# Kernel optimization log

Hardware: AMD Instinct MI355X
Metric: run time of the kernel (lower is better)

## Reference

```python
import jax, jax.numpy as jnp
import numpy as np

DIM = 64
N_EMBED = 1024
DECAY = 0.99
EPS = 1e-05
B, T = 2048, 128


def setup_inputs() -> dict:
    key = jax.random.key(0)
    k1, k2, k3 = jax.random.split(key, 3)
    x = jax.random.normal(k1, (B, T, DIM), dtype=jnp.float32)
    mask = jax.random.randint(k2, (B, T), 0, 2).astype(bool)
    embed = jax.random.normal(k3, (DIM, N_EMBED), dtype=jnp.float32)
    cluster_size = jnp.zeros((N_EMBED,), dtype=jnp.float32)
    embed_avg = embed  # buffer initialized as embed.clone()
    return {"input": x, "mask": mask, "embed": embed,
            "cluster_size": cluster_size, "embed_avg": embed_avg}


def reference(input, mask, embed, cluster_size, embed_avg):
    # --- nearest-codebook lookup ---
    flat = input.reshape(-1, DIM)                               # [N, D]
    dist = (jnp.sum(flat * flat, axis=1, keepdims=True)
            - 2.0 * flat @ embed
            + jnp.sum(embed * embed, axis=0, keepdims=True))    # [N, K]
    embed_ind = jnp.argmin(dist, axis=1)                        # [N]
    quantize = embed.T[embed_ind].reshape(input.shape)          # gather [N, D]
    # straight-through estimator
    quantize = input + jax.lax.stop_gradient(quantize - input)

    # --- masked MSE loss: mse over rows where ~mask, averaged over n_valid*DIM ---
    valid = (~mask).reshape(-1).astype(input.dtype)             # [N]
    n_valid = jnp.sum(valid)
    sq = jnp.sum((jax.lax.stop_gradient(quantize) - input).reshape(-1, DIM) ** 2, axis=1)
    loss = jnp.sum(sq * valid) / (n_valid * DIM)

    # --- EMA codebook update (training branch) ---
    counts = jnp.zeros((N_EMBED,), input.dtype).at[embed_ind].add(valid)
    embed_sum = jnp.zeros((N_EMBED, DIM), input.dtype).at[embed_ind].add(
        flat * valid[:, None]).T                                # [D, K]
    new_cluster_size = cluster_size * DECAY + (1.0 - DECAY) * counts
    new_embed_avg = embed_avg * DECAY + (1.0 - DECAY) * embed_sum
    total = jnp.sum(new_cluster_size)
    smoothed = (new_cluster_size + EPS) / (total + N_EMBED * EPS) * total
    new_embed = new_embed_avg / smoothed[None, :]
    return quantize, loss, new_embed, new_cluster_size, new_embed_avg
```

## Files before the change

### kernel.cpp

```cpp
#include <hip/hip_runtime.h>

typedef short short8 __attribute__((ext_vector_type(8)));
typedef float f32x16 __attribute__((ext_vector_type(16)));

#define DIMV   64
#define NEMB   1024
#define NROWS  262144
#define DECAYF 0.99f
#define OMDF   0.01f
#define EPSF   1e-5f
#define NSH    8

#define OQ   0
#define OL   16777216
#define OE   16777217
#define ONC  16842753
#define OA   16843777
#define OEH  16777216
#define OEL  (16777216 + 32768)

#define WS_E2     0
#define WS_CNT    1024
#define WS_ESUM   9216
#define WS_LOSSP  74752
#define WS_TOTAL  75776
#define WS_ET     75780
#define WS_KWV    141316
#define WS_BUCKET 272388

__device__ __forceinline__ unsigned short f2bf(float f) {
    unsigned u = __float_as_uint(f);
    u = u + 0x7FFFu + ((u >> 16) & 1u);
    return (unsigned short)(u >> 16);
}
__device__ __forceinline__ float bf2f(unsigned short h) {
    return __uint_as_float(((unsigned)h) << 16);
}

__global__ void vq_prep(const float* __restrict__ embed, float* __restrict__ et)
{
    int idx = blockIdx.x * 256 + threadIdx.x;
    int d = idx >> 10;
    int k = idx & (NEMB - 1);
    et[k * DIMV + d] = embed[idx];
}

__global__ void vq_e2(const float* __restrict__ et, float* __restrict__ e2)
{
    int k = blockIdx.x * 256 + threadIdx.x;
    const float4* ep = (const float4*)(et + k * DIMV);
    float s = 0.f;
    #pragma unroll
    for (int i = 0; i < 16; i++) {
        float4 v = ep[i];
        s = fmaf(v.x, v.x, fmaf(v.y, v.y, fmaf(v.z, v.z, fmaf(v.w, v.w, s))));
    }
    e2[k] = s;
}

__global__ void vq_prep_b(const float* __restrict__ embed,
                          unsigned short* __restrict__ eh,
                          unsigned short* __restrict__ el)
{
    int t = blockIdx.x * 256 + threadIdx.x;
    int j  = t & 7;
    int L  = (t >> 3) & 63;
    int s  = (t >> 9) & 3;
    int nt = t >> 11;
    int d    = s * 16 + (L >> 5) * 8 + j;
    int code = nt * 32 + (L & 31);
    float e = embed[d * NEMB + code];
    unsigned short hb = f2bf(e);
    eh[t] = hb;
    el[t] = f2bf(e - bf2f(hb));
}

__global__ __launch_bounds__(256, 2) void vq_main(
    const float* __restrict__ x, const int* __restrict__ mask,
    const unsigned short* __restrict__ eh, const unsigned short* __restrict__ el,
    const float* __restrict__ et, const float* __restrict__ e2g,
    float* __restrict__ out, unsigned short* __restrict__ kwv,
    float* __restrict__ loss_part)
{
    const int tid  = threadIdx.x;
    const int lane = tid & 63;
    const int wid  = tid >> 6;
    const int wbase = blockIdx.x * 256 + wid * 64;
    const int lm = lane & 31;
    const int lh = lane >> 5;

    __shared__ float lw[4];

    short8 ah[2][4], al[2][4];
    #pragma unroll
    for (int mt = 0; mt < 2; mt++) {
        const float* xr = x + (size_t)(wbase + mt * 32 + lm) * DIMV + lh * 8;
        #pragma unroll
        for (int s = 0; s < 4; s++) {
            const float* xp = xr + s * 16;
            #pragma unroll
            for (int j = 0; j < 8; j++) {
                float f = xp[j];
                unsigned short hb = f2bf(f);
                ah[mt][s][j] = (short)hb;
                al[mt][s][j] = (short)f2bf(f - bf2f(hb));
            }
        }
    }

    int b1[2][16], b2[2][16];
    #pragma unroll
    for (int mt = 0; mt < 2; mt++)
        #pragma unroll
        for (int r = 0; r < 16; r++) { b1[mt][r] = 0x7FFFFFFF; b2[mt][r] = 0x7FFFFFFF; }

    const short8* ehf = (const short8*)eh;
    const short8* elf = (const short8*)el;

    for (int nt = 0; nt < 32; nt++) {
        short8 bh[4], bl[4];
        #pragma unroll
        for (int s = 0; s < 4; s++) {
            bh[s] = ehf[(nt * 4 + s) * 64 + lane];
            bl[s] = elf[(nt * 4 + s) * 64 + lane];
        }
        const int   klane = nt * 32 + lm;
        const float e2s   = e2g[klane] * 2048.0f;

        f32x16 acc0, acc1;
        #pragma unroll
        for (int i = 0; i < 16; i++) { acc0[i] = 0.0f; acc1[i] = 0.0f; }

        #pragma unroll
        for (int s = 0; s < 4; s++) {
            acc0 = __builtin_amdgcn_mfma_f32_32x32x16_bf16(ah[0][s], bh[s], acc0, 0, 0, 0);
            acc1 = __builtin_amdgcn_mfma_f32_32x32x16_bf16(ah[1][s], bh[s], acc1, 0, 0, 0);
        }
        #pragma unroll
        for (int s = 0; s < 4; s++) {
            acc0 = __builtin_amdgcn_mfma_f32_32x32x16_bf16(ah[0][s], bl[s], acc0, 0, 0, 0);
            acc1 = __builtin_amdgcn_mfma_f32_32x32x16_bf16(ah[1][s], bl[s], acc1, 0, 0, 0);
        }
        #pragma unroll
        for (int s = 0; s < 4; s++) {
            acc0 = __builtin_amdgcn_mfma_f32_32x32x16_bf16(al[0][s], bh[s], acc0, 0, 0, 0);
            acc1 = __builtin_amdgcn_mfma_f32_32x32x16_bf16(al[1][s], bh[s], acc1, 0, 0, 0);
        }

        #pragma unroll
        for (int r = 0; r < 16; r++) {
            int q0   = (int)fmaf(acc0[r], -4096.0f, e2s);
            int key0 = (int)(((unsigned)q0) << 10) | klane;
            int lo0 = min(b1[0][r], key0), hi0 = max(b1[0][r], key0);
            b1[0][r] = lo0; b2[0][r] = min(b2[0][r], hi0);

            int q1   = (int)fmaf(acc1[r], -4096.0f, e2s);
            int key1 = (int)(((unsigned)q1) << 10) | klane;
            int lo1 = min(b1[1][r], key1), hi1 = max(b1[1][r], key1);
            b1[1][r] = lo1; b2[1][r] = min(b2[1][r], hi1);
        }
    }

    int sm1 = 0x7FFFFFFF, sm2 = 0x7FFFFFFF, sc = 1;
    unsigned long long hm = (lane < 32) ? 0xFFFFFFFFull : 0xFFFFFFFF00000000ull;
    #pragma unroll
    for (int mt = 0; mt < 2; mt++) {
        #pragma unroll
        for (int r = 0; r < 16; r++) {
            int v1 = b1[mt][r], v2 = b2[mt][r];
            #pragma unroll
            for (int m = 1; m <= 16; m <<= 1) {
                int o1 = __shfl_xor(v1, m, 64);
                int o2 = __shfl_xor(v2, m, 64);
                int lo = min(v1, o1), hi = max(v1, o1);
                v1 = lo;
                v2 = min(min(v2, o2), hi);
            }
            int thr = (v1 >> 10) + 41;
            bool in1 = (b1[mt][r] >> 10) <= thr;
            bool in2 = (b2[mt][r] >> 10) <= thr;
            unsigned long long B1 = __ballot(in1), B2 = __ballot(in2);
            int cnt = (int)__popcll(B1 & hm) + (int)__popcll(B2 & hm);
            int w1a = __shfl(v1, 0, 64),  w2a = __shfl(v2, 0, 64),  ca = __shfl(cnt, 0, 64);
            int w1b = __shfl(v1, 32, 64), w2b = __shfl(v2, 32, 64), cb = __shfl(cnt, 32, 64);
            int r0 = mt * 32 + (r & 3) + 8 * (r >> 2);
            if (lane == r0)     { sm1 = w1a; sm2 = w2a; sc = ca; }
            if (lane == r0 + 4) { sm1 = w1b; sm2 = w2b; sc = cb; }
        }
    }

    const int row = wbase + lane;
    int kw = sm1 & 1023;

    {
        unsigned long long fm = __ballot(sc >= 3);
        while (fm) {
            int j = __ffsll(fm) - 1; fm &= (fm - 1);
            const float4* xr = (const float4*)(x + (size_t)(wbase + j) * DIMV);
            float4 xb[16];
            float xb2 = 0.f;
            #pragma unroll
            for (int i = 0; i < 16; i++) {
                float4 v = xr[i];
                xb[i] = v;
                xb2 += v.x * v.x + v.y * v.y + v.z * v.z + v.w * v.w;
            }
            float bd = 3.4e38f; int bc = 0;
            for (int t = 0; t < 16; t++) {
                int c = lane + (t << 6);
                const float4* ep = (const float4*)(et + (c << 6));
                float ax = 0.f, ay = 0.f, az = 0.f, aw = 0.f;
                #pragma unroll 4
                for (int i = 0; i < 16; i++) {
                    float4 ev = ep[i];
                    ax = fmaf(xb[i].x, ev.x, ax);
                    ay = fmaf(xb[i].y, ev.y, ay);
                    az = fmaf(xb[i].z, ev.z, az);
                    aw = fmaf(xb[i].w, ev.w, aw);
                }
                float dot = (ax + ay) + (az + aw);
                float d = (xb2 - 2.0f * dot) + e2g[c];
                if (d < bd) { bd = d; bc = c; }
            }
            #pragma unroll
            for (int m = 1; m < 64; m <<= 1) {
                float od = __shfl_xor(bd, m, 64);
                int   oc = __shfl_xor(bc, m, 64);
                if (od < bd || (od == bd && oc < bc)) { bd = od; bc = oc; }
            }
            if (lane == j) kw = bc;
        }
    }

    float4 xv[16];
    {
        const float4* xp = (const float4*)(x + (size_t)row * DIMV);
        #pragma unroll
        for (int i = 0; i < 16; i++) xv[i] = xp[i];
    }

    if (sc == 2) {
        float x2 = 0.f;
        #pragma unroll
        for (int i = 0; i < 16; i++)
            x2 += xv[i].x * xv[i].x + xv[i].y * xv[i].y + xv[i].z * xv[i].z + xv[i].w * xv[i].w;

        auto fdist = [&](int k) -> float {
            const float4* ep = (const float4*)(et + (k << 6));
            float ax = 0.f, ay = 0.f, az = 0.f, aw = 0.f;
            #pragma unroll
            for (int i = 0; i < 16; i++) {
                float4 ev = ep[i];
                ax = fmaf(xv[i].x, ev.x, ax);
                ay = fmaf(xv[i].y, ev.y, ay);
                az = fmaf(xv[i].z, ev.z, az);
                aw = fmaf(xv[i].w, ev.w, aw);
            }
            float dot = (ax + ay) + (az + aw);
            return (x2 - 2.0f * dot) + e2g[k];
        };

        int k2 = sm2 & 1023;
        float d1 = fdist(kw);
        float d2 = fdist(k2);
        if (d2 < d1 || (d2 == d1 && k2 < kw)) kw = k2;
    }

    const bool valid = (mask[row] == 0);
    float sq = 0.f;
    float4* qp = (float4*)(out + OQ + (size_t)row * DIMV);
    const float4* erow = (const float4*)(et + (kw << 6));
    #pragma unroll
    for (int i = 0; i < 16; i++) {
        float4 xvv = xv[i];
        float4 ev  = erow[i];
        float q0 = xvv.x + (ev.x - xvv.x);
        float q1 = xvv.y + (ev.y - xvv.y);
        float q2 = xvv.z + (ev.z - xvv.z);
        float q3 = xvv.w + (ev.w - xvv.w);
        float4 q4 = {q0, q1, q2, q3};
        qp[i] = q4;
        float d0 = q0 - xvv.x, d1 = q1 - xvv.y, d2 = q2 - xvv.z, d3 = q3 - xvv.w;
        sq += d0 * d0 + d1 * d1 + d2 * d2 + d3 * d3;
    }

    kwv[row] = valid ? (unsigned short)kw : (unsigned short)0xFFFF;

    float v = valid ? sq : 0.0f;
    #pragma unroll
    for (int off = 32; off > 0; off >>= 1) v += __shfl_down(v, off, 64);
    if (lane == 0) lw[wid] = v;
    __syncthreads();
    if (tid == 0) loss_part[blockIdx.x] = (lw[0] + lw[1]) + (lw[2] + lw[3]);
}

__global__ __launch_bounds__(256) void vq_bucket(
    const unsigned short* __restrict__ kwv, const float* __restrict__ x,
    int* __restrict__ cnt, int* __restrict__ bucket,
    float* __restrict__ esum, int capS)
{
    int row = blockIdx.x * 256 + threadIdx.x;
    unsigned short c = kwv[row];
    if (c == 0xFFFFu) return;
    int s = blockIdx.x & (NSH - 1);
    int pos = atomicAdd(&cnt[(int)c + (s << 10)], 1);
    if (pos < capS) {
        bucket[((size_t)s * NEMB + (int)c) * capS + pos] = row;
    } else {
        const float* xr = x + (size_t)row * DIMV;
        float* ep = esum + ((int)c << 6);
        #pragma unroll 8
        for (int i = 0; i < DIMV; i++) atomicAdd(ep + i, xr[i]);
    }
}

__global__ __launch_bounds__(512) void vq_esum(
    const float* __restrict__ x, const int* __restrict__ cnt,
    const int* __restrict__ bucket, float* __restrict__ esum, int capS)
{
    const int tid  = threadIdx.x;
    const int lane = tid & 63;
    const int wid  = tid >> 6;
    const int c    = blockIdx.x;
    const int n    = min(cnt[c + (wid << 10)], capS);
    const int* bp  = bucket + ((size_t)wid * NEMB + c) * capS;
    __shared__ float part[8][64];

    float acc = 0.f;
    for (int i = 0; i < n; i += 8) {
        float tmp[8];
        if (i + 8 <= n) {
            int4 a = *(const int4*)(bp + i);
            int4 b = *(const int4*)(bp + i + 4);
            tmp[0] = x[(size_t)a.x * DIMV + lane];
            tmp[1] = x[(size_t)a.y * DIMV + lane];
            tmp[2] = x[(size_t)a.z * DIMV + lane];
            tmp[3] = x[(size_t)a.w * DIMV + lane];
            tmp[4] = x[(size_t)b.x * DIMV + lane];
            tmp[5] = x[(size_t)b.y * DIMV + lane];
            tmp[6] = x[(size_t)b.z * DIMV + lane];
            tmp[7] = x[(size_t)b.w * DIMV + lane];
        } else {
            #pragma unroll
            for (int k = 0; k < 8; k++) {
                int idx = i + k;
                tmp[k] = (idx < n) ? x[(size_t)bp[idx] * DIMV + lane] : 0.f;
            }
        }
        acc += ((tmp[0] + tmp[1]) + (tmp[2] + tmp[3]))
             + ((tmp[4] + tmp[5]) + (tmp[6] + tmp[7]));
    }

    part[wid][lane] = acc;
    __syncthreads();
    if (tid < 64) {
        float s = 0.f;
        #pragma unroll
        for (int w = 0; w < 8; w++) s += part[w][lane];
        esum[(c << 6) + lane] += s;
    }
}

__global__ __launch_bounds__(1024) void vq_finalA(
    const float* __restrict__ cluster_size, const int* __restrict__ cnt,
    const float* __restrict__ loss_part, float* __restrict__ out,
    float* __restrict__ total_ws)
{
    __shared__ float s1[1024];
    __shared__ float s2[1024];
    __shared__ float s3[1024];
    int k = threadIdx.x;
    int ci = 0;
    #pragma unroll
    for (int s = 0; s < NSH; s++) ci += cnt[k + (s << 10)];
    float c   = (float)ci;
    float ncs = cluster_size[k] * DECAYF + OMDF * c;
    out[ONC + k] = ncs;
    s1[k] = ncs; s2[k] = c; s3[k] = loss_part[k];
    __syncthreads();
    for (int off = 512; off > 0; off >>= 1) {
        if (k < off) { s1[k] += s1[k + off]; s2[k] += s2[k + off]; s3[k] += s3[k + off]; }
        __syncthreads();
    }
    if (k == 0) {
        total_ws[0] = s1[0];
        out[OL] = s3[0] / (s2[0] * (float)DIMV);
    }
}

__global__ void vq_finalB(const float* __restrict__ embed_avg,
                          const float* __restrict__ esum,
                          float* __restrict__ out,
                          const float* __restrict__ total_ws)
{
    int idx = blockIdx.x * 256 + threadIdx.x;
    int k = idx & (NEMB - 1);
    int d = idx >> 10;
    float avg = embed_avg[idx] * DECAYF + OMDF * esum[(k << 6) + d];
    out[OA + idx] = avg;
    float ncs   = out[ONC + k];
    float total = *total_ws;
    float sm = (ncs + EPSF) / (total + (float)NEMB * EPSF) * total;
    out[OE + idx] = avg / sm;
}

extern "C" void kernel_launch(void* const* d_in, const int* in_sizes, int n_in,
                              void* d_out, int out_size, void* d_ws, size_t ws_size,
                              hipStream_t stream)
{
    const float* x            = (const float*)d_in[0];
    const int*   mask         = (const int*)d_in[1];
    const float* embed        = (const float*)d_in[2];
    const float* cluster_size = (const float*)d_in[3];
    const float* embed_avg    = (const float*)d_in[4];
    float* out = (float*)d_out;
    float* ws  = (float*)d_ws;

    unsigned short* eh     = (unsigned short*)(out + OEH);
    unsigned short* el     = (unsigned short*)(out + OEL);
    unsigned short* kwv    = (unsigned short*)(ws + WS_KWV);
    int*            cnt    = (int*)(ws + WS_CNT);
    int*            bucket = (int*)(ws + WS_BUCKET);

    int capS = 0;
    size_t avail = ws_size / sizeof(float);
    if (avail > (size_t)WS_BUCKET) {
        size_t per = (avail - (size_t)WS_BUCKET) / ((size_t)NEMB * NSH);
        if (per > 768) per = 768;
        capS = (int)per & ~7;
    }

    hipMemsetAsync(ws + WS_CNT, 0, (size_t)(WS_LOSSP - WS_CNT) * sizeof(float), stream);

    vq_prep<<<65536 / 256, 256, 0, stream>>>(embed, ws + WS_ET);
    vq_e2<<<NEMB / 256, 256, 0, stream>>>(ws + WS_ET, ws + WS_E2);
    vq_prep_b<<<65536 / 256, 256, 0, stream>>>(embed, eh, el);
    vq_main<<<NROWS / 256, 256, 0, stream>>>(x, mask, eh, el, ws + WS_ET, ws + WS_E2,
                                             out, kwv, ws + WS_LOSSP);
    vq_bucket<<<NROWS / 256, 256, 0, stream>>>(kwv, x, cnt, bucket, ws + WS_ESUM, capS);
    vq_esum<<<NEMB, 512, 0, stream>>>(x, cnt, bucket, ws + WS_ESUM, capS);
    vq_finalA<<<1, 1024, 0, stream>>>(cluster_size, cnt, ws + WS_LOSSP,
                                      out, ws + WS_TOTAL);
    vq_finalB<<<65536 / 256, 256, 0, stream>>>(embed_avg, ws + WS_ESUM, out, ws + WS_TOTAL);
}
```

Baseline: 378.4 us.

## Halve rows per wave in vq_main to raise occupancy; fuse prep kernels

```diff
diff --git a/kernel.cpp b/kernel.cpp
--- a/kernel.cpp
+++ b/kernel.cpp
@@ -23,10 +23,10 @@
 #define WS_CNT    1024
 #define WS_ESUM   9216
 #define WS_LOSSP  74752
-#define WS_TOTAL  75776
-#define WS_ET     75780
-#define WS_KWV    141316
-#define WS_BUCKET 272388
+#define WS_TOTAL  76800
+#define WS_ET     76804
+#define WS_KWV    142340
+#define WS_BUCKET 273412
 
 __device__ __forceinline__ unsigned short f2bf(float f) {
     unsigned u = __float_as_uint(f);
@@ -37,45 +37,39 @@
     return __uint_as_float(((unsigned)h) << 16);
 }
 
-__global__ void vq_prep(const float* __restrict__ embed, float* __restrict__ et)
-{
-    int idx = blockIdx.x * 256 + threadIdx.x;
-    int d = idx >> 10;
-    int k = idx & (NEMB - 1);
-    et[k * DIMV + d] = embed[idx];
-}
-
-__global__ void vq_e2(const float* __restrict__ et, float* __restrict__ e2)
-{
-    int k = blockIdx.x * 256 + threadIdx.x;
-    const float4* ep = (const float4*)(et + k * DIMV);
-    float s = 0.f;
-    #pragma unroll
-    for (int i = 0; i < 16; i++) {
-        float4 v = ep[i];
-        s = fmaf(v.x, v.x, fmaf(v.y, v.y, fmaf(v.z, v.z, fmaf(v.w, v.w, s))));
-    }
-    e2[k] = s;
-}
-
-__global__ void vq_prep_b(const float* __restrict__ embed,
-                          unsigned short* __restrict__ eh,
-                          unsigned short* __restrict__ el)
+__global__ void vq_prep(const float* __restrict__ embed, float* __restrict__ et,
+                        unsigned short* __restrict__ eh, unsigned short* __restrict__ el)
 {
     int t = blockIdx.x * 256 + threadIdx.x;
+    int d = t >> 10;
+    int k = t & (NEMB - 1);
+    et[k * DIMV + d] = embed[t];
     int j  = t & 7;
     int L  = (t >> 3) & 63;
     int s  = (t >> 9) & 3;
     int nt = t >> 11;
-    int d    = s * 16 + (L >> 5) * 8 + j;
+    int db   = s * 16 + (L >> 5) * 8 + j;
     int code = nt * 32 + (L & 31);
-    float e = embed[d * NEMB + code];
+    float e = embed[db * NEMB + code];
     unsigned short hb = f2bf(e);
     eh[t] = hb;
     el[t] = f2bf(e - bf2f(hb));
 }
 
-__global__ __launch_bounds__(256, 2) void vq_main(
+__global__ void vq_e2(const float* __restrict__ et, float* __restrict__ e2)
+{
+    int k = blockIdx.x * 256 + threadIdx.x;
+    const float4* ep = (const float4*)(et + k * DIMV);
+    float s = 0.f;
+    #pragma unroll
+    for (int i = 0; i < 16; i++) {
+        float4 v = ep[i];
+        s = fmaf(v.x, v.x, fmaf(v.y, v.y, fmaf(v.z, v.z, fmaf(v.w, v.w, s))));
+    }
+    e2[k] = s;
+}
+
+__global__ __launch_bounds__(256, 5) void vq_main(
     const float* __restrict__ x, const int* __restrict__ mask,
     const unsigned short* __restrict__ eh, const unsigned short* __restrict__ el,
     const float* __restrict__ et, const float* __restrict__ e2g,
@@ -85,16 +79,15 @@
     const int tid  = threadIdx.x;
     const int lane = tid & 63;
     const int wid  = tid >> 6;
-    const int wbase = blockIdx.x * 256 + wid * 64;
+    const int wbase = blockIdx.x * 128 + wid * 32;
     const int lm = lane & 31;
     const int lh = lane >> 5;
 
     __shared__ float lw[4];
 
-    short8 ah[2][4], al[2][4];
-    #pragma unroll
-    for (int mt = 0; mt < 2; mt++) {
-        const float* xr = x + (size_t)(wbase + mt * 32 + lm) * DIMV + lh * 8;
+    short8 ah[4], al[4];
+    {
+        const float* xr = x + (size_t)(wbase + lm) * DIMV + lh * 8;
         #pragma unroll
         for (int s = 0; s < 4; s++) {
             const float* xp = xr + s * 16;
@@ -102,17 +95,15 @@
             for (int j = 0; j < 8; j++) {
                 float f = xp[j];
                 unsigned short hb = f2bf(f);
-                ah[mt][s][j] = (short)hb;
-                al[mt][s][j] = (short)f2bf(f - bf2f(hb));
-            }
-        }
-    }
-
-    int b1[2][16], b2[2][16];
-    #pragma unroll
-    for (int mt = 0; mt < 2; mt++)
-        #pragma unroll
-        for (int r = 0; r < 16; r++) { b1[mt][r] = 0x7FFFFFFF; b2[mt][r] = 0x7FFFFFFF; }
+                ah[s][j] = (short)hb;
+                al[s][j] = (short)f2bf(f - bf2f(hb));
+            }
+        }
+    }
+
+    int b1[16], b2[16];
+    #pragma unroll
+    for (int r = 0; r < 16; r++) { b1[r] = 0x7FFFFFFF; b2[r] = 0x7FFFFFFF; }
 
     const short8* ehf = (const short8*)eh;
     const short8* elf = (const short8*)el;
@@ -127,69 +118,54 @@
         const int   klane = nt * 32 + lm;
         const float e2s   = e2g[klane] * 2048.0f;
 
-        f32x16 acc0, acc1;
-        #pragma unroll
-        for (int i = 0; i < 16; i++) { acc0[i] = 0.0f; acc1[i] = 0.0f; }
-
-        #pragma unroll
-        for (int s = 0; s < 4; s++) {
-            acc0 = __builtin_amdgcn_mfma_f32_32x32x16_bf16(ah[0][s], bh[s], acc0, 0, 0, 0);
-            acc1 = __builtin_amdgcn_mfma_f32_32x32x16_bf16(ah[1][s], bh[s], acc1, 0, 0, 0);
-        }
-        #pragma unroll
-        for (int s = 0; s < 4; s++) {
-            acc0 = __builtin_amdgcn_mfma_f32_32x32x16_bf16(ah[0][s], bl[s], acc0, 0, 0, 0);
-            acc1 = __builtin_amdgcn_mfma_f32_32x32x16_bf16(ah[1][s], bl[s], acc1, 0, 0, 0);
-        }
-        #pragma unroll
-        for (int s = 0; s < 4; s++) {
-            acc0 = __builtin_amdgcn_mfma_f32_32x32x16_bf16(al[0][s], bh[s], acc0, 0, 0, 0);
-            acc1 = __builtin_amdgcn_mfma_f32_32x32x16_bf16(al[1][s], bh[s], acc1, 0, 0, 0);
-        }
+        f32x16 acc;
+        #pragma unroll
+        for (int i = 0; i < 16; i++) acc[i] = 0.0f;
+
+        #pragma unroll
+        for (int s = 0; s < 4; s++)
+            acc = __builtin_amdgcn_mfma_f32_32x32x16_bf16(ah[s], bh[s], acc, 0, 0, 0);
+        #pragma unroll
+        for (int s = 0; s < 4; s++)
+            acc = __builtin_amdgcn_mfma_f32_32x32x16_bf16(ah[s], bl[s], acc, 0, 0, 0);
+        #pragma unroll
+        for (int s = 0; s < 4; s++)
+            acc = __builtin_amdgcn_mfma_f32_32x32x16_bf16(al[s], bh[s], acc, 0, 0, 0);
 
         #pragma unroll
         for (int r = 0; r < 16; r++) {
-            int q0   = (int)fmaf(acc0[r], -4096.0f, e2s);
-            int key0 = (int)(((unsigned)q0) << 10) | klane;
-            int lo0 = min(b1[0][r], key0), hi0 = max(b1[0][r], key0);
-            b1[0][r] = lo0; b2[0][r] = min(b2[0][r], hi0);
-
-            int q1   = (int)fmaf(acc1[r], -4096.0f, e2s);
-            int key1 = (int)(((unsigned)q1) << 10) | klane;
-            int lo1 = min(b1[1][r], key1), hi1 = max(b1[1][r], key1);
-            b1[1][r] = lo1; b2[1][r] = min(b2[1][r], hi1);
+            int q   = (int)fmaf(acc[r], -4096.0f, e2s);
+            int key = (int)(((unsigned)q) << 10) | klane;
+            int lo = min(b1[r], key), hi = max(b1[r], key);
+            b1[r] = lo; b2[r] = min(b2[r], hi);
         }
     }
 
     int sm1 = 0x7FFFFFFF, sm2 = 0x7FFFFFFF, sc = 1;
     unsigned long long hm = (lane < 32) ? 0xFFFFFFFFull : 0xFFFFFFFF00000000ull;
     #pragma unroll
-    for (int mt = 0; mt < 2; mt++) {
-        #pragma unroll
-        for (int r = 0; r < 16; r++) {
-            int v1 = b1[mt][r], v2 = b2[mt][r];
-            #pragma unroll
-            for (int m = 1; m <= 16; m <<= 1) {
-                int o1 = __shfl_xor(v1, m, 64);
-                int o2 = __shfl_xor(v2, m, 64);
-                int lo = min(v1, o1), hi = max(v1, o1);
-                v1 = lo;
-                v2 = min(min(v2, o2), hi);
-            }
-            int thr = (v1 >> 10) + 41;
-            bool in1 = (b1[mt][r] >> 10) <= thr;
-            bool in2 = (b2[mt][r] >> 10) <= thr;
-            unsigned long long B1 = __ballot(in1), B2 = __ballot(in2);
-            int cnt = (int)__popcll(B1 & hm) + (int)__popcll(B2 & hm);
-            int w1a = __shfl(v1, 0, 64),  w2a = __shfl(v2, 0, 64),  ca = __shfl(cnt, 0, 64);
-            int w1b = __shfl(v1, 32, 64), w2b = __shfl(v2, 32, 64), cb = __shfl(cnt, 32, 64);
-            int r0 = mt * 32 + (r & 3) + 8 * (r >> 2);
-            if (lane == r0)     { sm1 = w1a; sm2 = w2a; sc = ca; }
-            if (lane == r0 + 4) { sm1 = w1b; sm2 = w2b; sc = cb; }
-        }
-    }
-
-    const int row = wbase + lane;
+    for (int r = 0; r < 16; r++) {
+        int v1 = b1[r], v2 = b2[r];
+        #pragma unroll
+        for (int m = 1; m <= 16; m <<= 1) {
+            int o1 = __shfl_xor(v1, m, 64);
+            int o2 = __shfl_xor(v2, m, 64);
+            int lo = min(v1, o1), hi = max(v1, o1);
+            v1 = lo;
+            v2 = min(min(v2, o2), hi);
+        }
+        int thr = (v1 >> 10) + 41;
+        bool in1 = (b1[r] >> 10) <= thr;
+        bool in2 = (b2[r] >> 10) <= thr;
+        unsigned long long B1 = __ballot(in1), B2 = __ballot(in2);
+        int cnt = (int)__popcll(B1 & hm) + (int)__popcll(B2 & hm);
+        int w1a = __shfl(v1, 0, 64),  w2a = __shfl(v2, 0, 64),  ca = __shfl(cnt, 0, 64);
+        int w1b = __shfl(v1, 32, 64), w2b = __shfl(v2, 32, 64), cb = __shfl(cnt, 32, 64);
+        int r0 = (r & 3) + 8 * (r >> 2);
+        if (lane == r0)     { sm1 = w1a; sm2 = w2a; sc = ca; }
+        if (lane == r0 + 4) { sm1 = w1b; sm2 = w2b; sc = cb; }
+    }
+
     int kw = sm1 & 1023;
 
     {
@@ -232,47 +208,56 @@
         }
     }
 
-    float4 xv[16];
+    kw  = __shfl(kw,  lm, 64);
+    sm2 = __shfl(sm2, lm, 64);
+    sc  = __shfl(sc,  lm, 64);
+
+    const int row = wbase + lm;
+    const bool valid = (mask[row] == 0);
+
+    float4 xc[8];
     {
-        const float4* xp = (const float4*)(x + (size_t)row * DIMV);
-        #pragma unroll
-        for (int i = 0; i < 16; i++) xv[i] = xp[i];
+        const float4* xp = (const float4*)(x + (size_t)row * DIMV + lh * 32);
+        #pragma unroll
+        for (int i = 0; i < 8; i++) xc[i] = xp[i];
     }
 
     if (sc == 2) {
-        float x2 = 0.f;
-        #pragma unroll
-        for (int i = 0; i < 16; i++)
-            x2 += xv[i].x * xv[i].x + xv[i].y * xv[i].y + xv[i].z * xv[i].z + xv[i].w * xv[i].w;
-
-        auto fdist = [&](int k) -> float {
-            const float4* ep = (const float4*)(et + (k << 6));
+        float x2h = 0.f;
+        #pragma unroll
+        for (int i = 0; i < 8; i++)
+            x2h += xc[i].x * xc[i].x + xc[i].y * xc[i].y + xc[i].z * xc[i].z + xc[i].w * xc[i].w;
+
+        auto doth = [&](int k) -> float {
+            const float4* ep = (const float4*)(et + (k << 6) + lh * 32);
             float ax = 0.f, ay = 0.f, az = 0.f, aw = 0.f;
             #pragma unroll
-            for (int i = 0; i < 16; i++) {
+            for (int i = 0; i < 8; i++) {
                 float4 ev = ep[i];
-                ax = fmaf(xv[i].x, ev.x, ax);
-                ay = fmaf(xv[i].y, ev.y, ay);
-                az = fmaf(xv[i].z, ev.z, az);
-                aw = fmaf(xv[i].w, ev.w, aw);
-            }
-            float dot = (ax + ay) + (az + aw);
-            return (x2 - 2.0f * dot) + e2g[k];
+                ax = fmaf(xc[i].x, ev.x, ax);
+                ay = fmaf(xc[i].y, ev.y, ay);
+                az = fmaf(xc[i].z, ev.z, az);
+                aw = fmaf(xc[i].w, ev.w, aw);
+            }
+            return (ax + ay) + (az + aw);
         };
 
         int k2 = sm2 & 1023;
-        float d1 = fdist(kw);
-        float d2 = fdist(k2);
+        float p1 = x2h - 2.0f * doth(kw);
+        float p2 = x2h - 2.0f * doth(k2);
+        p1 += __shfl_xor(p1, 32, 64);
+        p2 += __shfl_xor(p2, 32, 64);
+        float d1 = p1 + e2g[kw];
+        float d2 = p2 + e2g[k2];
         if (d2 < d1 || (d2 == d1 && k2 < kw)) kw = k2;
     }
 
-    const bool valid = (mask[row] == 0);
-    float sq = 0.f;
-    float4* qp = (float4*)(out + OQ + (size_t)row * DIMV);
-    const float4* erow = (const float4*)(et + (kw << 6));
-    #pragma unroll
-    for (int i = 0; i < 16; i++) {
-        float4 xvv = xv[i];
+    float sqh = 0.f;
+    float4* qp = (float4*)(out + OQ + (size_t)row * DIMV + lh * 32);
+    const float4* erow = (const float4*)(et + (kw << 6) + lh * 32);
+    #pragma unroll
+    for (int i = 0; i < 8; i++) {
+        float4 xvv = xc[i];
         float4 ev  = erow[i];
         float q0 = xvv.x + (ev.x - xvv.x);
         float q1 = xvv.y + (ev.y - xvv.y);
@@ -281,12 +266,12 @@
         float4 q4 = {q0, q1, q2, q3};
         qp[i] = q4;
         float d0 = q0 - xvv.x, d1 = q1 - xvv.y, d2 = q2 - xvv.z, d3 = q3 - xvv.w;
-        sq += d0 * d0 + d1 * d1 + d2 * d2 + d3 * d3;
-    }
-
-    kwv[row] = valid ? (unsigned short)kw : (unsigned short)0xFFFF;
-
-    float v = valid ? sq : 0.0f;
+        sqh += d0 * d0 + d1 * d1 + d2 * d2 + d3 * d3;
+    }
+
+    if (lh == 0) kwv[row] = valid ? (unsigned short)kw : (unsigned short)0xFFFF;
+
+    float v = valid ? sqh : 0.0f;
     #pragma unroll
     for (int off = 32; off > 0; off >>= 1) v += __shfl_down(v, off, 64);
     if (lane == 0) lw[wid] = v;
@@ -376,7 +361,7 @@
     float c   = (float)ci;
     float ncs = cluster_size[k] * DECAYF + OMDF * c;
     out[ONC + k] = ncs;
-    s1[k] = ncs; s2[k] = c; s3[k] = loss_part[k];
+    s1[k] = ncs; s2[k] = c; s3[k] = loss_part[k] + loss_part[k + 1024];
     __syncthreads();
     for (int off = 512; off > 0; off >>= 1) {
         if (k < off) { s1[k] += s1[k + off]; s2[k] += s2[k + off]; s3[k] += s3[k + off]; }
@@ -432,10 +417,9 @@
 
     hipMemsetAsync(ws + WS_CNT, 0, (size_t)(WS_LOSSP - WS_CNT) * sizeof(float), stream);
 
-    vq_prep<<<65536 / 256, 256, 0, stream>>>(embed, ws + WS_ET);
+    vq_prep<<<65536 / 256, 256, 0, stream>>>(embed, ws + WS_ET, eh, el);
     vq_e2<<<NEMB / 256, 256, 0, stream>>>(ws + WS_ET, ws + WS_E2);
-    vq_prep_b<<<65536 / 256, 256, 0, stream>>>(embed, eh, el);
-    vq_main<<<NROWS / 256, 256, 0, stream>>>(x, mask, eh, el, ws + WS_ET, ws + WS_E2,
+    vq_main<<<NROWS / 128, 256, 0, stream>>>(x, mask, eh, el, ws + WS_ET, ws + WS_E2,
                                              out, kwv, ws + WS_LOSSP);
     vq_bucket<<<NROWS / 256, 256, 0, stream>>>(kwv, x, cnt, bucket, ws + WS_ESUM, capS);
     vq_esum<<<NEMB, 512, 0, stream>>>(x, cnt, bucket, ws + WS_ESUM, capS);
```

Measured after the change: 503.7 us. 33.1% more time.
